# Kernel tuning notes

Measured on AMD Instinct MI355X. Metric: run time of the kernel, lower is better.

## Reference

```python
import jax, jax.numpy as jnp
import numpy as np

DIM = 180
HEADS = 6
WIN = 12
NGS = 2304          # num_gs_seed -> gs len
SQ = 48             # sqrt(num_gs_seed)
B = 64              # window-batch
TABLE = (2 * max(SQ, WIN) - 1) ** 2  # 9025 rows in bias table


def _rel_pos_index():
    # Mirrors the torch __init__ buffer construction (np.unique gives the
    # deterministic sorted-unique indexing the original intends).
    cs = (np.indices((SQ, SQ)) + 0.5) * WIN          # [2, SQ, SQ]
    ct = (np.indices((WIN, WIN)) + 0.5) * SQ
    d = cs.reshape(2, -1)[:, :, None] - ct.reshape(2, -1)[:, None, :]
    _, inv = np.unique(d.flatten(), return_inverse=True)
    idx = inv.reshape(d.shape).astype(np.int64)
    idx[0] *= idx.max()
    return jnp.asarray(idx.sum(0), dtype=jnp.int32)


def setup_inputs() -> dict:
    key = jax.random.key(0)
    ks = jax.random.split(key, 12)
    std = 0.02
    d = DIM
    inp = {
        "gs": jax.random.normal(ks[0], (B, NGS, d), dtype=jnp.float32),
        "feat": jax.random.normal(ks[1], (B, WIN * WIN, d), dtype=jnp.float32),
        "Wq": jax.random.normal(ks[2], (d, d), dtype=jnp.float32) * std,
        "bq": jnp.zeros((d,), dtype=jnp.float32),
        "Wk": jax.random.normal(ks[3], (d, d), dtype=jnp.float32) * std,
        "bk": jnp.zeros((d,), dtype=jnp.float32),
        "Wv": jax.random.normal(ks[4], (d, d), dtype=jnp.float32) * std,
        "bv": jnp.zeros((d,), dtype=jnp.float32),
        "Wp": jax.random.normal(ks[5], (d, d), dtype=jnp.float32) * std,
        "bp": jnp.zeros((d,), dtype=jnp.float32),
        "bias_table": jax.random.normal(ks[6], (TABLE, HEADS), dtype=jnp.float32) * std,
        "rel_pos_index": _rel_pos_index(),
    }
    return inp


def reference(gs, feat, Wq, bq, Wk, bk, Wv, bv, Wp, bp, bias_table, rel_pos_index):
    b, ng, c = gs.shape
    n = feat.shape[1]
    hd = c // HEADS
    scale = hd ** (-0.5)

    q = (gs @ Wq + bq).reshape(b, ng, HEADS, hd).transpose(0, 2, 1, 3) * scale  # [b,H,ng,hd]
    k = (feat @ Wk + bk).reshape(b, n, HEADS, hd).transpose(0, 2, 1, 3)          # [b,H,n,hd]
    v = (feat @ Wv + bv).reshape(b, n, HEADS, hd).transpose(0, 2, 1, 3)

    attn = jnp.einsum('bhqd,bhkd->bhqk', q, k)                                    # [b,H,ng,n]
    bias = bias_table[rel_pos_index]                                              # [ng,n,H]
    attn = attn + jnp.transpose(bias, (2, 0, 1))[None]                            # broadcast over b
    attn = jax.nn.softmax(attn, axis=-1)

    x = jnp.einsum('bhqk,bhkd->bhqd', attn, v)                                    # [b,H,ng,hd]
    x = x.transpose(0, 2, 1, 3).reshape(b, ng, c)
    return x @ Wp + bp
```

## Files before the change

kernel.cpp:

```cpp
#include <hip/hip_runtime.h>

#define DIM   180
#define HEADS 6
#define HD    30
#define NKEY  144
#define NGS   2304
#define BATCH 64
#define TQ    64
#define QT    36
#define WPAD  192
#define SXS   200
#define SPS   152
#define KROW  40
#define VROW  144
#define KB_STRIDE (NKEY * KROW)
#define VB_STRIDE (32 * VROW)

typedef unsigned short u16;
typedef short v8s __attribute__((ext_vector_type(8)));
typedef float v4f __attribute__((ext_vector_type(4)));

__device__ __forceinline__ float bf2f(u16 u) {
    union { unsigned int i; float f; } w; w.i = ((unsigned int)u) << 16; return w.f;
}
__device__ __forceinline__ u16 f2bf(float f) {
    union { float f; unsigned int i; } w; w.f = f;
    unsigned int r = w.i + 0x7fffu + ((w.i >> 16) & 1u);
    return (u16)(r >> 16);
}
__device__ __forceinline__ unsigned cvt_pk_bf16(float lo, float hi) {
    unsigned r;
    asm("v_cvt_pk_bf16_f32 %0, %1, %2" : "=v"(r) : "v"(lo), "v"(hi));
    return r;
}
__device__ __forceinline__ uint2 pack4(const v4f& x) {
    return make_uint2(cvt_pk_bf16(x[0], x[1]), cvt_pk_bf16(x[2], x[3]));
}


__global__ __launch_bounds__(256) void wt_prep_kernel(
    const float* __restrict__ Wq, const float* __restrict__ Wp,
    u16* __restrict__ WqT, u16* __restrict__ WpT) {
    int idx = blockIdx.x * 256 + threadIdx.x;
    int sel = idx >= WPAD * WPAD;
    int rr  = sel ? idx - WPAD * WPAD : idx;
    int j = rr / WPAD, k = rr - j * WPAD;
    float v;
    if (!sel) {
        v = (j < DIM && k < DIM) ? Wq[k * DIM + j] : 0.f;
        WqT[j * WPAD + k] = f2bf(v);
    } else {
        int h = k >> 5, dd = k & 31;
        v = (j < DIM && dd < HD) ? Wp[(h * HD + dd) * DIM + j] : 0.f;
        WpT[j * WPAD + k] = f2bf(v);
    }
}

__global__ __launch_bounds__(256) void gather_bias_kernel(
    const float* __restrict__ table, const int* __restrict__ rpi,
    u16* __restrict__ biasCT) {
    const float LOG2E = 1.4426950408889634f;
    int i = blockIdx.x * 256 + threadIdx.x;
    int lane = i & 63;
    int tile = i >> 6;
    int t = tile % 9;
    int rem = tile / 9;
    int g = rem % 144;
    int h = rem / 144;
    int q  = 16 * g + (lane & 15);
    int n0 = 16 * t + (lane >> 4) * 4;
    const int4 rr = *(const int4*)&rpi[q * NKEY + n0];
    unsigned lo = (unsigned)f2bf(table[rr.x * HEADS + h] * LOG2E) |
                  ((unsigned)f2bf(table[rr.y * HEADS + h] * LOG2E) << 16);
    unsigned hi = (unsigned)f2bf(table[rr.z * HEADS + h] * LOG2E) |
                  ((unsigned)f2bf(table[rr.w * HEADS + h] * LOG2E) << 16);
    ((uint2*)biasCT)[i] = make_uint2(lo, hi);
}

__global__ __launch_bounds__(256) void kv_proj_kernel(
    const float* __restrict__ feat,
    const float* __restrict__ Wk, const float* __restrict__ bk,
    const float* __restrict__ Wv, const float* __restrict__ bv,
    u16* __restrict__ Kb, u16* __restrict__ VbT) {
    __shared__ float sF[16 * DIM];
    int b  = blockIdx.x / 9;
    int n0 = (blockIdx.x % 9) * 16;
    int tid = threadIdx.x;
    {
        const float4* src = (const float4*)(feat + (size_t)(b * NKEY + n0) * DIM);
        float4* dst = (float4*)sF;
        for (int i = tid; i < 16 * 45; i += 256) dst[i] = src[i];
    }
    __syncthreads();
    int j = tid;
    if (j < DIM) {
        float ak[16], av[16];
#pragma unroll
        for (int r = 0; r < 16; ++r) { ak[r] = 0.f; av[r] = 0.f; }
        const float4* sF4 = (const float4*)sF;
        for (int kc = 0; kc < 45; ++kc) {
            int kk = kc * 4;
            float wk0 = Wk[(kk + 0) * DIM + j], wk1 = Wk[(kk + 1) * DIM + j];
            float wk2 = Wk[(kk + 2) * DIM + j], wk3 = Wk[(kk + 3) * DIM + j];
            float wv0 = Wv[(kk + 0) * DIM + j], wv1 = Wv[(kk + 1) * DIM + j];
            float wv2 = Wv[(kk + 2) * DIM + j], wv3 = Wv[(kk + 3) * DIM + j];
#pragma unroll
            for (int r = 0; r < 16; ++r) {
                float4 g = sF4[r * 45 + kc];
                ak[r] = fmaf(g.x, wk0, ak[r]); ak[r] = fmaf(g.y, wk1, ak[r]);
                ak[r] = fmaf(g.z, wk2, ak[r]); ak[r] = fmaf(g.w, wk3, ak[r]);
                av[r] = fmaf(g.x, wv0, av[r]); av[r] = fmaf(g.y, wv1, av[r]);
                av[r] = fmaf(g.z, wv2, av[r]); av[r] = fmaf(g.w, wv3, av[r]);
            }
        }
        int h = j / HD, d = j - HD * h;
        u16* kp = Kb  + (size_t)(b * HEADS + h) * KB_STRIDE;
        u16* vp = VbT + (size_t)(b * HEADS + h) * VB_STRIDE;
        float bkj = bk[j], bvj = bv[j];
#pragma unroll
        for (int r = 0; r < 16; ++r) {
            kp[(n0 + r) * KROW + d] = f2bf(ak[r] + bkj);
            vp[d * VROW + n0 + r]   = f2bf(av[r] + bvj);
        }
    }
}

__global__ __launch_bounds__(256, 3) void attn_kernel(
    const float* __restrict__ gs,
    const u16* __restrict__ WqT, const float* __restrict__ bq,
    const u16* __restrict__ WpT, const float* __restrict__ bp,
    const u16* __restrict__ Kb, const u16* __restrict__ VbT,
    const u16* __restrict__ biasCT, float* __restrict__ out) {

    __shared__ u16 sXQ[TQ * SXS];
    __shared__ u16 sP[TQ * SPS];

    const int tid  = threadIdx.x;
    const int w    = tid >> 6;
    const int lane = tid & 63;
    const int l15  = tid & 15;
    const int quad = (tid >> 4) & 3;
    const int bid  = blockIdx.x;
    const int i8   = bid >> 3;
    const int qt   = i8 >> 3;
    const int b    = (bid & 7) * 8 + (i8 & 7);
    const int q0   = qt * TQ;
    const float SCALE = 0.18257418583505536f * 1.4426950408889634f;

    {
        const float4* src = (const float4*)(gs + (size_t)(b * NGS + q0) * DIM);
        for (int i = tid; i < TQ * 45; i += 256) {
            int row = i / 45, c = i - row * 45;
            float4 g = src[row * 45 + c];
            *(uint2*)&sXQ[row * SXS + c * 4] =
                make_uint2(cvt_pk_bf16(g.x, g.y), cvt_pk_bf16(g.z, g.w));
        }
        for (int i = tid; i < TQ * 16; i += 256)
            sXQ[(i >> 4) * SXS + 180 + (i & 15)] = 0;
    }
    __syncthreads();

    v4f qacc[12];
#pragma unroll
    for (int i = 0; i < 12; ++i) qacc[i] = (v4f){0.f, 0.f, 0.f, 0.f};
    for (int kt = 0; kt < 6; ++kt) {
        v8s A[4];
#pragma unroll
        for (int m = 0; m < 4; ++m)
            A[m] = *(const v8s*)&sXQ[(16 * m + l15) * SXS + kt * 32 + quad * 8];
#pragma unroll
        for (int jj = 0; jj < 3; ++jj) {
            v8s B = *(const v8s*)&WqT[(size_t)((3 * w + jj) * 16 + l15) * WPAD +
                                      kt * 32 + quad * 8];
#pragma unroll
            for (int m = 0; m < 4; ++m)
                qacc[jj * 4 + m] = __builtin_amdgcn_mfma_f32_16x16x32_bf16(
                    A[m], B, qacc[jj * 4 + m], 0, 0, 0);
        }
    }
    __syncthreads();
#pragma unroll
    for (int jj = 0; jj < 3; ++jj) {
        int j = (3 * w + jj) * 16 + l15;
        if (j < DIM) {
            int h = j / HD;
            int pos = j + 2 * h;
            float bqj = bq[j];
#pragma unroll
            for (int m = 0; m < 4; ++m)
#pragma unroll
                for (int r = 0; r < 4; ++r) {
                    float v = (qacc[jj * 4 + m][r] + bqj) * SCALE;
                    sXQ[(16 * m + quad * 4 + r) * SXS + pos] =
                        (u16)cvt_pk_bf16(v, v);
                }
        }
    }
    for (int i = tid; i < TQ * 12; i += 256) {
        int row = i / 12, c = i - row * 12;
        sXQ[row * SXS + (c >> 1) * 32 + 30 + (c & 1)] = 0;
    }
    __syncthreads();

    for (int h = 0; h < HEADS; ++h) {
        const u16* kp = Kb  + (size_t)(b * HEADS + h) * KB_STRIDE;
        const u16* vp = VbT + (size_t)(b * HEADS + h) * VB_STRIDE;

        v8s qa = *(const v8s*)&sXQ[(16 * w + l15) * SXS + h * 32 + quad * 8];

        const u16* bgt = biasCT +
            ((size_t)((h * 144 + (qt * 4 + w)) * 9) * 256) + lane * 4;
        uint2 bb[9];
#pragma unroll
        for (int t = 0; t < 9; ++t) bb[t] = *(const uint2*)(bgt + t * 256);
        v8s kb[9];
#pragma unroll
        for (int t = 0; t < 9; ++t)
            kb[t] = *(const v8s*)&kp[(16 * t + l15) * KROW + quad * 8];

        v4f la[9];
#pragma unroll
        for (int t = 0; t < 9; ++t) {
            la[t][0] = bf2f((u16)(bb[t].x & 0xffff));
            la[t][1] = bf2f((u16)(bb[t].x >> 16));
            la[t][2] = bf2f((u16)(bb[t].y & 0xffff));
            la[t][3] = bf2f((u16)(bb[t].y >> 16));
        }
#pragma unroll
        for (int t = 0; t < 9; ++t)
            la[t] = __builtin_amdgcn_mfma_f32_16x16x32_bf16(kb[t], qa, la[t], 0, 0, 0);

        v8s va0[5], va1[5];
#pragma unroll
        for (int kt = 0; kt < 5; ++kt) {
            int co = (kt == 4 && quad >= 2) ? 0 : kt * 32 + quad * 8;
            va0[kt] = *(const v8s*)&vp[l15 * VROW + co];
            va1[kt] = *(const v8s*)&vp[(16 + l15) * VROW + co];
        }

        float m = la[0][0];
#pragma unroll
        for (int t = 0; t < 9; ++t)
#pragma unroll
            for (int r = 0; r < 4; ++r) m = fmaxf(m, la[t][r]);
        m = fmaxf(m, __shfl_xor(m, 16));
        m = fmaxf(m, __shfl_xor(m, 32));
        float s = 0.f;
#pragma unroll
        for (int t = 0; t < 9; ++t)
#pragma unroll
            for (int r = 0; r < 4; ++r) {
                la[t][r] = __builtin_amdgcn_exp2f(la[t][r] - m);
                s += la[t][r];
            }
        s += __shfl_xor(s, 16);
        s += __shfl_xor(s, 32);
        float inv = 1.f / s;

#pragma unroll
        for (int t = 0; t < 9; ++t)
            *(uint2*)&sP[(16 * w + l15) * SPS + 16 * t + quad * 4] =
                make_uint2(cvt_pk_bf16(la[t][0], la[t][1]),
                           cvt_pk_bf16(la[t][2], la[t][3]));

        v4f x0 = (v4f){0.f, 0.f, 0.f, 0.f}, x1 = x0;
#pragma unroll
        for (int kt = 0; kt < 5; ++kt) {
            v8s pa = (v8s){0, 0, 0, 0, 0, 0, 0, 0};
            if (!(kt == 4 && quad >= 2))
                pa = *(const v8s*)&sP[(16 * w + l15) * SPS + kt * 32 + quad * 8];
            x0 = __builtin_amdgcn_mfma_f32_16x16x32_bf16(va0[kt], pa, x0, 0, 0, 0);
            x1 = __builtin_amdgcn_mfma_f32_16x16x32_bf16(va1[kt], pa, x1, 0, 0, 0);
        }
        v4f y0, y1;
#pragma unroll
        for (int r = 0; r < 4; ++r) { y0[r] = x0[r] * inv; y1[r] = x1[r] * inv; }
        *(uint2*)&sXQ[(16 * w + l15) * SXS + h * 32 + quad * 4]      = pack4(y0);
        *(uint2*)&sXQ[(16 * w + l15) * SXS + h * 32 + 16 + quad * 4] = pack4(y1);
    }
    __syncthreads();

    {
        v4f acc[12];
#pragma unroll
        for (int i = 0; i < 12; ++i) acc[i] = (v4f){0.f, 0.f, 0.f, 0.f};
        for (int kt = 0; kt < 6; ++kt) {
            v8s A[4];
#pragma unroll
            for (int m = 0; m < 4; ++m)
                A[m] = *(const v8s*)&sXQ[(16 * m + l15) * SXS + kt * 32 + quad * 8];
#pragma unroll
            for (int jj = 0; jj < 3; ++jj) {
                v8s B = *(const v8s*)&WpT[(size_t)((3 * w + jj) * 16 + l15) * WPAD +
                                          kt * 32 + quad * 8];
#pragma unroll
                for (int m = 0; m < 4; ++m)
                    acc[jj * 4 + m] = __builtin_amdgcn_mfma_f32_16x16x32_bf16(
                        A[m], B, acc[jj * 4 + m], 0, 0, 0);
            }
        }
#pragma unroll
        for (int jj = 0; jj < 3; ++jj) {
            int j = (3 * w + jj) * 16 + l15;
            if (j < DIM) {
                float bpj = bp[j];
#pragma unroll
                for (int m = 0; m < 4; ++m)
#pragma unroll
                    for (int r = 0; r < 4; ++r)
                        out[(size_t)(b * NGS + q0 + 16 * m + quad * 4 + r) * DIM + j] =
                            acc[jj * 4 + m][r] + bpj;
            }
        }
    }
}

extern "C" void kernel_launch(void* const* d_in, const int* in_sizes, int n_in,
                              void* d_out, int out_size, void* d_ws, size_t ws_size,
                              hipStream_t stream) {
    const float* gs    = (const float*)d_in[0];
    const float* feat  = (const float*)d_in[1];
    const float* Wq    = (const float*)d_in[2];
    const float* bq    = (const float*)d_in[3];
    const float* Wk    = (const float*)d_in[4];
    const float* bk    = (const float*)d_in[5];
    const float* Wv    = (const float*)d_in[6];
    const float* bv    = (const float*)d_in[7];
    const float* Wp    = (const float*)d_in[8];
    const float* bp    = (const float*)d_in[9];
    const float* table = (const float*)d_in[10];
    const int*   rpi   = (const int*)d_in[11];
    float* out = (float*)d_out;

    u16* WqT    = (u16*)d_ws;
    u16* WpT    = WqT + WPAD * WPAD;
    u16* Kb     = WpT + WPAD * WPAD;
    u16* VbT    = Kb  + (size_t)BATCH * HEADS * KB_STRIDE;
    u16* biasCT = VbT + (size_t)BATCH * HEADS * VB_STRIDE;

    size_t zero_bytes = (size_t)BATCH * HEADS * (KB_STRIDE + VB_STRIDE) * sizeof(u16);
    hipMemsetAsync(Kb, 0, zero_bytes, stream);

    wt_prep_kernel<<<dim3(2 * WPAD * WPAD / 256), dim3(256), 0, stream>>>(Wq, Wp, WqT, WpT);
    gather_bias_kernel<<<dim3(HEADS * 144 * 9 * 64 / 256), dim3(256), 0, stream>>>(
        table, rpi, biasCT);
    kv_proj_kernel<<<dim3(BATCH * 9), dim3(256), 0, stream>>>(feat, Wk, bk, Wv, bv, Kb, VbT);
    attn_kernel<<<dim3(BATCH * QT), dim3(256), 0, stream>>>(
        gs, WqT, bq, WpT, bp, Kb, VbT, biasCT, out);
}
```

Before: 376.8 us.

## Stage per-head K and V into LDS with direct global-to-LDS loads

Each head's K and V tiles are now copied once per block into shared memory with global_load_lds 16-byte transfers, instead of every wave loading its own copy from global memory into registers. The K staging buffer is reused for the softmax probabilities, and the K row pitch and P row pitch are shrunk to unpadded sizes so the tiles fit and copy contiguously. This cuts redundant global/L2 traffic across the four waves. In exchange it adds three block barriers per head and removes padding, which may cause LDS bank conflicts.

```diff
diff --git a/kernel.cpp b/kernel.cpp
--- a/kernel.cpp
+++ b/kernel.cpp
@@ -10,8 +10,8 @@
 #define QT    36
 #define WPAD  192
 #define SXS   200
-#define SPS   152
-#define KROW  40
+#define SPS   144
+#define KROW  32
 #define VROW  144
 #define KB_STRIDE (NKEY * KROW)
 #define VB_STRIDE (32 * VROW)
@@ -35,6 +35,11 @@
 }
 __device__ __forceinline__ uint2 pack4(const v4f& x) {
     return make_uint2(cvt_pk_bf16(x[0], x[1]), cvt_pk_bf16(x[2], x[3]));
+}
+__device__ __forceinline__ void gload_lds16(const u16* g, u16* l) {
+    __builtin_amdgcn_global_load_lds(
+        (const __attribute__((address_space(1))) unsigned int*)g,
+        (__attribute__((address_space(3))) unsigned int*)l, 16, 0, 0);
 }
 
 
@@ -133,7 +138,8 @@
     const u16* __restrict__ biasCT, float* __restrict__ out) {
 
     __shared__ u16 sXQ[TQ * SXS];
-    __shared__ u16 sP[TQ * SPS];
+    __shared__ u16 sV[32 * VROW];
+    __shared__ u16 sPK[TQ * SPS];
 
     const int tid  = threadIdx.x;
     const int w    = tid >> 6;
@@ -203,20 +209,23 @@
     __syncthreads();
 
     for (int h = 0; h < HEADS; ++h) {
-        const u16* kp = Kb  + (size_t)(b * HEADS + h) * KB_STRIDE;
-        const u16* vp = VbT + (size_t)(b * HEADS + h) * VB_STRIDE;
-
-        v8s qa = *(const v8s*)&sXQ[(16 * w + l15) * SXS + h * 32 + quad * 8];
-
+        if (h) __syncthreads();
+
+        {
+            const u16* kg = Kb  + (size_t)(b * HEADS + h) * KB_STRIDE;
+            const u16* vg = VbT + (size_t)(b * HEADS + h) * VB_STRIDE;
+            for (int i = tid; i < 576; i += 256) gload_lds16(kg + i * 8, sPK + i * 8);
+            for (int i = tid; i < 576; i += 256) gload_lds16(vg + i * 8, sV + i * 8);
+        }
         const u16* bgt = biasCT +
             ((size_t)((h * 144 + (qt * 4 + w)) * 9) * 256) + lane * 4;
         uint2 bb[9];
 #pragma unroll
         for (int t = 0; t < 9; ++t) bb[t] = *(const uint2*)(bgt + t * 256);
-        v8s kb[9];
-#pragma unroll
-        for (int t = 0; t < 9; ++t)
-            kb[t] = *(const v8s*)&kp[(16 * t + l15) * KROW + quad * 8];
+
+        v8s qa = *(const v8s*)&sXQ[(16 * w + l15) * SXS + h * 32 + quad * 8];
+
+        __syncthreads();
 
         v4f la[9];
 #pragma unroll
@@ -227,16 +236,12 @@
             la[t][3] = bf2f((u16)(bb[t].y >> 16));
         }
 #pragma unroll
-        for (int t = 0; t < 9; ++t)
-            la[t] = __builtin_amdgcn_mfma_f32_16x16x32_bf16(kb[t], qa, la[t], 0, 0, 0);
-
-        v8s va0[5], va1[5];
-#pragma unroll
-        for (int kt = 0; kt < 5; ++kt) {
-            int co = (kt == 4 && quad >= 2) ? 0 : kt * 32 + quad * 8;
-            va0[kt] = *(const v8s*)&vp[l15 * VROW + co];
-            va1[kt] = *(const v8s*)&vp[(16 + l15) * VROW + co];
-        }
+        for (int t = 0; t < 9; ++t) {
+            v8s kb = *(const v8s*)&sPK[(16 * t + l15) * KROW + quad * 8];
+            la[t] = __builtin_amdgcn_mfma_f32_16x16x32_bf16(kb, qa, la[t], 0, 0, 0);
+        }
+
+        __syncthreads();
 
         float m = la[0][0];
 #pragma unroll
@@ -259,7 +264,7 @@
 
 #pragma unroll
         for (int t = 0; t < 9; ++t)
-            *(uint2*)&sP[(16 * w + l15) * SPS + 16 * t + quad * 4] =
+            *(uint2*)&sPK[(16 * w + l15) * SPS + 16 * t + quad * 4] =
                 make_uint2(cvt_pk_bf16(la[t][0], la[t][1]),
                            cvt_pk_bf16(la[t][2], la[t][3]));
 
@@ -267,10 +272,15 @@
 #pragma unroll
         for (int kt = 0; kt < 5; ++kt) {
             v8s pa = (v8s){0, 0, 0, 0, 0, 0, 0, 0};
-            if (!(kt == 4 && quad >= 2))
-                pa = *(const v8s*)&sP[(16 * w + l15) * SPS + kt * 32 + quad * 8];
-            x0 = __builtin_amdgcn_mfma_f32_16x16x32_bf16(va0[kt], pa, x0, 0, 0, 0);
-            x1 = __builtin_amdgcn_mfma_f32_16x16x32_bf16(va1[kt], pa, x1, 0, 0, 0);
+            v8s a0 = pa, a1 = pa;
+            if (!(kt == 4 && quad >= 2)) {
+                int co = kt * 32 + quad * 8;
+                pa = *(const v8s*)&sPK[(16 * w + l15) * SPS + co];
+                a0 = *(const v8s*)&sV[l15 * VROW + co];
+                a1 = *(const v8s*)&sV[(16 + l15) * VROW + co];
+            }
+            x0 = __builtin_amdgcn_mfma_f32_16x16x32_bf16(a0, pa, x0, 0, 0, 0);
+            x1 = __builtin_amdgcn_mfma_f32_16x16x32_bf16(a1, pa, x1, 0, 0, 0);
         }
         v4f y0, y1;
 #pragma unroll
```

Result: faster. 365.3 us (-3.1%).
